# Kernel optimization log

Hardware: AMD Instinct MI355X
Metric: run time of the kernel (lower is better)

## Reference

```python
import jax, jax.numpy as jnp
import numpy as np
import math

# static config
NH, HD, HID = 16, 128, 2048
ROT = 64            # head_dim * partial_rotary_factor(0.5)
EPS = 1e-6
GROUPS = 8
CHUNK = 64
THETA = 10000.0
LAYER_IDX, N_LAYERS = 1, 32
B, S = 2, 2048


def _base_slopes(n):
    # power-of-two branch of HF ALiBi slopes
    start = 2 ** (-(2 ** (-(math.log2(n) - 3))))
    return [start * (start ** i) for i in range(n)]

# per-head log-decay (negative): slope = -base * (1 - (l-1)/(L-1) + 1e-5)
SLOPE = jnp.asarray(
    -np.array(_base_slopes(NH), dtype=np.float32)
    * (1.0 - (LAYER_IDX - 1) / (N_LAYERS - 1) + 1e-5),
    dtype=jnp.float32)  # [NH]


def _rmsnorm(x, w):
    return x * jax.lax.rsqrt(jnp.mean(x * x, axis=-1, keepdims=True) + EPS) * w


def _partial_rope(x, positions):
    # x: [B,S,NH,HD]; neox-style rotary on first ROT dims, rest passthrough
    half = ROT // 2
    inv_freq = 1.0 / (THETA ** (jnp.arange(half, dtype=jnp.float32) / half))
    ang = positions.astype(jnp.float32)[:, None] * inv_freq       # [S, half]
    cos = jnp.cos(ang)[None, :, None, :]
    sin = jnp.sin(ang)[None, :, None, :]
    x1, x2, rest = x[..., :half], x[..., half:ROT], x[..., ROT:]
    return jnp.concatenate(
        [x1 * cos - x2 * sin, x2 * cos + x1 * sin, rest], axis=-1)


def setup_inputs() -> dict:
    key = jax.random.key(0)
    ks = jax.random.split(key, 4)
    return {
        'positions': jnp.arange(S, dtype=jnp.int32),
        'hidden_states': jax.random.normal(ks[0], (B, S, HID), jnp.float32),
        'recurrent_state': jnp.zeros((B, NH, HD, HD), jnp.float32),
        'w_qkv': jax.random.normal(ks[1], (HID, 3 * NH * HD), jnp.float32) * 0.02,
        'w_g': jax.random.normal(ks[2], (HID, NH * HD), jnp.float32) * 0.02,
        'w_dense': jax.random.normal(ks[3], (NH * HD, HID), jnp.float32) * 0.02,
        'q_norm_w': jnp.ones((HD,), jnp.float32),
        'k_norm_w': jnp.ones((HD,), jnp.float32),
        'g_norm_w': jnp.ones((NH * HD,), jnp.float32),
    }


def reference(positions, hidden_states, recurrent_state, w_qkv, w_g, w_dense,
              q_norm_w, k_norm_w, g_norm_w):
    # fused QKV projection
    qkv = hidden_states @ w_qkv                       # [B,S,3*NH*HD]
    q, k, v = jnp.split(qkv, 3, axis=-1)
    q = q.reshape(B, S, NH, HD)
    k = k.reshape(B, S, NH, HD)
    v = v.reshape(B, S, NH, HD)

    # QK RMSNorm then partial rotary
    q = _partial_rope(_rmsnorm(q, q_norm_w), positions)
    k = _partial_rope(_rmsnorm(k, k_norm_w), positions)

    # chunked ALiBi-decayed linear attention:
    #   S_t = lam * S_{t-1} + k_t v_t^T ; o_t = q_t S_t, lam = exp(slope)
    NC = S // CHUNK
    qc = q.reshape(B, NC, CHUNK, NH, HD).transpose(1, 0, 3, 2, 4)  # [NC,B,NH,C,HD]
    kc = k.reshape(B, NC, CHUNK, NH, HD).transpose(1, 0, 3, 2, 4)
    vc = v.reshape(B, NC, CHUNK, NH, HD).transpose(1, 0, 3, 2, 4)

    t = jnp.arange(CHUNK, dtype=jnp.float32)
    # intra-chunk causal decay mask lam^(i-j), i>=j: [NH,C,C]
    dec_mask = jnp.where(t[:, None] >= t[None, :],
                         jnp.exp(SLOPE[:, None, None] * (t[:, None] - t[None, :])),
                         0.0)
    q_dec = jnp.exp(SLOPE[:, None] * (t[None, :] + 1.0))            # [NH,C] lam^(i+1)
    k_dec = jnp.exp(SLOPE[:, None] * (CHUNK - 1.0 - t[None, :]))    # [NH,C] lam^(C-1-j)
    lam_C = jnp.exp(SLOPE * CHUNK)                                   # [NH]

    def step(state, inp):
        qb, kb, vb = inp                                  # [B,NH,C,HD]
        scores = jnp.einsum('bhid,bhjd->bhij', qb, kb) * dec_mask[None]
        o_intra = jnp.einsum('bhij,bhjd->bhid', scores, vb)
        o_inter = jnp.einsum('bhid,bhde->bhie', qb * q_dec[None, :, :, None], state)
        new_state = (state * lam_C[None, :, None, None]
                     + jnp.einsum('bhjd,bhje->bhde', kb * k_dec[None, :, :, None], vb))
        return new_state, o_intra + o_inter

    _, o = jax.lax.scan(step, recurrent_state, (qc, kc, vc))  # o: [NC,B,NH,C,HD]
    o = o.transpose(1, 0, 3, 2, 4).reshape(B, S, NH * HD)

    # GroupRMSNorm on attention output, sigmoid gate, output projection
    og = o.reshape(B, S, GROUPS, (NH * HD) // GROUPS)
    og = og * jax.lax.rsqrt(jnp.mean(og * og, axis=-1, keepdims=True) + EPS)
    o = og.reshape(B, S, NH * HD) * g_norm_w
    o = o * jax.nn.sigmoid(hidden_states @ w_g)
    return o @ w_dense
```

## Files before the change

### kernel.cpp

```cpp
#include <hip/hip_runtime.h>
#include <hip/hip_bf16.h>
#include <math.h>

#define NH   16
#define HD   128
#define HID  2048
#define NKV  6144
#define B_   2
#define S_   2048
#define NC   32
#define CHUNK_ 64
#define GROUPS_ 8

typedef __bf16 bf16_t;
typedef bf16_t bf16x8 __attribute__((ext_vector_type(8)));
typedef float  f32x4  __attribute__((ext_vector_type(4)));

__device__ __forceinline__ float b2f(unsigned int u) {
    union { unsigned int u; float f; } c; c.u = (u & 0xffffu) << 16; return c.f;
}
__device__ __forceinline__ unsigned int f2b(float f) {
    union { float f; unsigned int u; } c; c.f = f;
    unsigned int u = c.u;
    return (u + 0x7fffu + ((u >> 16) & 1u)) >> 16;
}

#define GLOAD_LDS16(gp, lp) __builtin_amdgcn_global_load_lds(                     \
    (const __attribute__((address_space(1))) void*)(gp),                          \
    (__attribute__((address_space(3))) void*)(lp), 16, 0, 0)

__global__ __launch_bounds__(256) void cvt_bf16(const float* __restrict__ in,
                                                unsigned short* __restrict__ out, int n8)
{
    int i = blockIdx.x * 256 + threadIdx.x;
    if (i >= n8) return;
    const float4* p = (const float4*)in + (size_t)i * 2;
    float4 a = p[0], b = p[1];
    uint4 o;
    o.x = f2b(a.x) | (f2b(a.y) << 16);
    o.y = f2b(a.z) | (f2b(a.w) << 16);
    o.z = f2b(b.x) | (f2b(b.y) << 16);
    o.w = f2b(b.z) | (f2b(b.w) << 16);
    ((uint4*)out)[i] = o;
}

__global__ __launch_bounds__(256) void transpose_cvt(const float* __restrict__ in,
                                                     unsigned short* __restrict__ out,
                                                     int Kdim, int Ndim)
{
    __shared__ float tile[32][33];
    int ntx = Ndim >> 5;
    int bx = blockIdx.x % ntx;
    int by = blockIdx.x / ntx;
    int lx = threadIdx.x & 31, ly = threadIdx.x >> 5;
    int r0 = by * 32, c0 = bx * 32;
    #pragma unroll
    for (int r = 0; r < 4; ++r)
        tile[ly + r * 8][lx] = in[(size_t)(r0 + ly + r * 8) * Ndim + c0 + lx];
    __syncthreads();
    #pragma unroll
    for (int r = 0; r < 4; ++r)
        out[(size_t)(c0 + ly + r * 8) * Kdim + r0 + lx] = (unsigned short)f2b(tile[lx][ly + r * 8]);
}

__global__ __launch_bounds__(256) void pack_b(const float* __restrict__ in,
                                              unsigned short* __restrict__ out, int Ndim)
{
    __shared__ float tile[32][33];
    int ntx = Ndim >> 5;
    int bx = blockIdx.x % ntx;
    int by = blockIdx.x / ntx;
    int lx = threadIdx.x & 31, ly = threadIdx.x >> 5;
    int r0 = by * 32, c0 = bx * 32;
    #pragma unroll
    for (int r = 0; r < 4; ++r)
        tile[ly + r * 8][lx] = in[(size_t)(r0 + ly + r * 8) * Ndim + c0 + lx];
    __syncthreads();
    int quad = (lx >> 3) & 3;
    int e    = lx & 7;
    #pragma unroll
    for (int r = 0; r < 4; ++r) {
        int n = c0 + ly + r * 8;
        int n16 = n >> 4, l16 = n & 15;
        out[((size_t)(n16 * 64 + by) << 9) + (quad * 16 + l16) * 8 + e] =
            (unsigned short)f2b(tile[lx][ly + r * 8]);
    }
}


__device__ __forceinline__ void ld_fr4(bf16x8 (&d)[4][2], const bf16_t* b, int s0, int ri) {
    #pragma unroll
    for (int i = 0; i < 4; ++i)
        #pragma unroll
        for (int k = 0; k < 2; ++k)
            d[i][k] = *(const bf16x8*)(b + (((s0 + i) * 2 + k) << 9) + ri);
}
__device__ __forceinline__ void mfma_quad(f32x4 (&a)[4][2], const bf16x8 (&af)[4][2],
                                          const bf16x8 (&bv)[2][2]) {
    #pragma unroll
    for (int mt = 0; mt < 4; ++mt)
        #pragma unroll
        for (int nt = 0; nt < 2; ++nt)
            #pragma unroll
            for (int ks = 0; ks < 2; ++ks)
                a[mt][nt] = __builtin_amdgcn_mfma_f32_16x16x32_bf16(af[mt][ks], bv[nt][ks], a[mt][nt], 0, 0, 0);
}
__device__ __forceinline__ void load_bfrag(bf16x8 (&d)[2][2][2], const bf16_t* Bp,
                                           int n16b, int tt, int lane8) {
    #pragma unroll
    for (int nh = 0; nh < 2; ++nh)
        #pragma unroll
        for (int nt = 0; nt < 2; ++nt)
            #pragma unroll
            for (int ks = 0; ks < 2; ++ks)
                d[nh][nt][ks] = *(const bf16x8*)(Bp +
                    ((size_t)((n16b + nh * 8 + nt) * 64 + tt * 2 + ks) << 9) + lane8);
}

#define BAR()     asm volatile("s_barrier" ::: "memory")
#define VMCNT0()  asm volatile("s_waitcnt vmcnt(0)" ::: "memory")

__global__ __launch_bounds__(512, 2) void gemm_qg_256(const bf16_t* __restrict__ A,
                                                      const bf16_t* __restrict__ Bp,
                                                      unsigned short* __restrict__ Cq,
                                                      unsigned short* __restrict__ Cg)
{
    __shared__ bf16_t Asm[2][2][8192];
    const int K  = HID;
    const int NT = K / 64;

    int tid  = threadIdx.x;
    int wave = tid >> 6, lane = tid & 63;
    int wm = wave >> 2, wn = wave & 3;
    int l16 = lane & 15, quad = lane >> 4;
    int wm4 = wm * 4;
    int lane8 = lane * 8;

    int bid = blockIdx.x;
    int xcd = bid & 7, idx = bid >> 3;
    int by  = (xcd >> 2) * 8 + (idx >> 3);
    int bx  = (xcd & 3) * 8 + (idx & 7);

    int n16b = bx * 16 + wn * 2;

    int rd_in = ((l16 << 5) | (quad << 3)) ^ (((l16 >> 3) & 1) << 4);

    int ch = lane ^ ((lane & 32) >> 4);
    int rr = ch >> 2;
    int cc = (ch & 3) * 8;

    const bf16_t* aSrc0 = A + (size_t)(by * 256 +       wave * 16 + rr) * K + cc;
    const bf16_t* aSrc1 = A + (size_t)(by * 256 + 128 + wave * 16 + rr) * K + cc;

#define STAGE_A(h, t) do {                                                        \
        const bf16_t* _g = ((h) ? aSrc1 : aSrc0) + (size_t)(t) * 64;              \
        bf16_t* _l = &Asm[(t) & 1][(h)][wave * 1024 + lane * 8];                  \
        GLOAD_LDS16(_g,      _l);                                                 \
        GLOAD_LDS16(_g + 32, _l + 512); } while (0)

    f32x4 acc[2][2][4][2];
    #pragma unroll
    for (int a0 = 0; a0 < 2; ++a0)
        #pragma unroll
        for (int a1 = 0; a1 < 2; ++a1)
            #pragma unroll
            for (int a2 = 0; a2 < 4; ++a2)
                #pragma unroll
                for (int a3 = 0; a3 < 2; ++a3) { f32x4 z = {0.f,0.f,0.f,0.f}; acc[a0][a1][a2][a3] = z; }

    bf16x8 af[4][2];
    bf16x8 bfA[2][2][2], bfB[2][2][2];

    load_bfrag(bfA, Bp, n16b, 0, lane8);
    STAGE_A(0, 0); STAGE_A(1, 0);
    VMCNT0();
    BAR();

#define QG_TILE(t, BFC, BFN) do {                                                 \
        const int buf_ = (t) & 1;                                                 \
        load_bfrag(BFN, Bp, n16b, (t) + 1, lane8);                                \
        STAGE_A(0, (t) + 1); STAGE_A(1, (t) + 1);                                 \
        ld_fr4(af, &Asm[buf_][0][0], wm4, rd_in);                                 \
        mfma_quad(acc[0][0], af, BFC[0]);                                         \
        mfma_quad(acc[0][1], af, BFC[1]);                                         \
        ld_fr4(af, &Asm[buf_][1][0], wm4, rd_in);                                 \
        mfma_quad(acc[1][1], af, BFC[1]);                                         \
        mfma_quad(acc[1][0], af, BFC[0]);                                         \
        VMCNT0();                                                                 \
        BAR(); } while (0)

    for (int t = 0; t < NT - 2; t += 2) {
        QG_TILE(t,     bfA, bfB);
        QG_TILE(t + 1, bfB, bfA);
    }
    QG_TILE(NT - 2, bfA, bfB);
    {
        ld_fr4(af, &Asm[1][0][0], wm4, rd_in);
        mfma_quad(acc[0][0], af, bfB[0]);
        mfma_quad(acc[0][1], af, bfB[1]);
        ld_fr4(af, &Asm[1][1][0], wm4, rd_in);
        mfma_quad(acc[1][1], af, bfB[1]);
        mfma_quad(acc[1][0], af, bfB[0]);
    }
#undef QG_TILE
#undef STAGE_A

    unsigned short* Cc; int Nn, colbase;
    if (bx < 24) { Cc = Cq; Nn = NKV; colbase = bx * 256; }
    else         { Cc = Cg; Nn = HID; colbase = bx * 256 - NKV; }
    int row0 = by * 256 + wm * 64 + quad * 4;
    int col0 = colbase + wn * 32 + l16;
    #pragma unroll
    for (int mh = 0; mh < 2; ++mh)
        #pragma unroll
        for (int nh = 0; nh < 2; ++nh)
            #pragma unroll
            for (int mt = 0; mt < 4; ++mt)
                #pragma unroll
                for (int nt = 0; nt < 2; ++nt) {
                    int col = col0 + nh * 128 + nt * 16;
                    #pragma unroll
                    for (int r = 0; r < 4; ++r) {
                        int row = row0 + mh * 128 + mt * 16 + r;
                        Cc[(size_t)row * Nn + col] = (unsigned short)f2b(acc[mh][nh][mt][nt][r]);
                    }
                }
}

__global__ __launch_bounds__(256, 2) void gemm_out_128(const bf16_t* __restrict__ A,
                                                       const bf16_t* __restrict__ Bt,
                                                       float* __restrict__ C)
{
    __shared__ bf16_t As[2][4096];
    __shared__ bf16_t Bs[2][4096];
    const int K  = HID;
    const int NT = K / 32;

    int tid  = threadIdx.x;
    int wave = tid >> 6, lane = tid & 63;
    int wm2 = wave >> 1, wn2 = wave & 1;
    int l16 = lane & 15, quad = lane >> 4;
    int w2 = wave * 2;

    int bid = blockIdx.x;
    int xcd = bid & 7, idx = bid >> 3;
    int by  = (xcd >> 1) * 8 + (idx >> 3);
    int bx  = (xcd & 1) * 8 + (idx & 7);

    int rd_in = ((l16 << 5) | (quad << 3)) ^ (((l16 >> 3) & 1) << 4);
    int ch = lane ^ ((lane & 32) >> 4);
    int rr = ch >> 2;
    int cc = (ch & 3) * 8;

    const bf16_t* aSrc = A  + (size_t)(by * 128 + w2 * 16 + rr) * K + cc;
    const bf16_t* bSrc = Bt + (size_t)(bx * 128 + w2 * 16 + rr) * K + cc;

#define OSTAGE(t) do {                                                            \
        const int nb_ = (t) & 1;                                                  \
        const bf16_t* _ga = aSrc + (size_t)(t) * 32;                              \
        const bf16_t* _gb = bSrc + (size_t)(t) * 32;                              \
        GLOAD_LDS16(_ga,                  &As[nb_][w2 * 512 + lane * 8]);         \
        GLOAD_LDS16(_ga + (size_t)16 * K, &As[nb_][w2 * 512 + 512 + lane * 8]);   \
        GLOAD_LDS16(_gb,                  &Bs[nb_][w2 * 512 + lane * 8]);         \
        GLOAD_LDS16(_gb + (size_t)16 * K, &Bs[nb_][w2 * 512 + 512 + lane * 8]); } while (0)

    f32x4 acc[4][4];
    #pragma unroll
    for (int i = 0; i < 4; ++i)
        #pragma unroll
        for (int j = 0; j < 4; ++j) { f32x4 z = {0.f,0.f,0.f,0.f}; acc[i][j] = z; }

#define OCOMP(t) do {                                                             \
        const int b_ = (t) & 1;                                                   \
        bf16x8 af_[4], bf_[4];                                                    \
        _Pragma("unroll")                                                         \
        for (int i = 0; i < 4; ++i)                                               \
            af_[i] = *(const bf16x8*)(&As[b_][((wm2 * 4 + i) << 9) + rd_in]);     \
        _Pragma("unroll")                                                         \
        for (int j = 0; j < 4; ++j)                                               \
            bf_[j] = *(const bf16x8*)(&Bs[b_][((wn2 * 4 + j) << 9) + rd_in]);     \
        _Pragma("unroll")                                                         \
        for (int i = 0; i < 4; ++i)                                               \
            _Pragma("unroll")                                                     \
            for (int j = 0; j < 4; ++j)                                           \
                acc[i][j] = __builtin_amdgcn_mfma_f32_16x16x32_bf16(af_[i], bf_[j], acc[i][j], 0, 0, 0); } while (0)

    OSTAGE(0);
    VMCNT0();
    BAR();
    #pragma unroll 2
    for (int t = 0; t < NT - 1; ++t) {
        OSTAGE(t + 1);
        OCOMP(t);
        VMCNT0();
        BAR();
    }
    OCOMP(NT - 1);
#undef OSTAGE
#undef OCOMP

    #pragma unroll
    for (int i = 0; i < 4; ++i)
        #pragma unroll
        for (int j = 0; j < 4; ++j) {
            int col = bx * 128 + wn2 * 64 + j * 16 + l16;
            #pragma unroll
            for (int r = 0; r < 4; ++r) {
                int row = by * 128 + wm2 * 64 + i * 16 + quad * 4 + r;
                C[(size_t)row * HID + col] = acc[i][j][r];
            }
        }
}

__global__ __launch_bounds__(256) void norm_rope(unsigned short* __restrict__ qkv,
                                                 const int* __restrict__ positions,
                                                 const float* __restrict__ qw,
                                                 const float* __restrict__ kw)
{
    int bs = blockIdx.x;
    int s  = bs & (S_ - 1);
    int tid = threadIdx.x;
    int l16 = tid & 15;
    unsigned short* base = qkv + (size_t)bs * NKV;
    float pos = (float)positions[s];

    #pragma unroll
    for (int p = 0; p < 2; ++p) {
        int rr = p * 16 + (tid >> 4);
        int qk = rr >> 4;
        int h  = rr & 15;
        unsigned short* row = base + qk * HID + h * HD;
        const float* w = qk ? kw : qw;
        uint4 v = *(const uint4*)(row + l16 * 8);
        float x[8];
        x[0] = b2f(v.x); x[1] = b2f(v.x >> 16);
        x[2] = b2f(v.y); x[3] = b2f(v.y >> 16);
        x[4] = b2f(v.z); x[5] = b2f(v.z >> 16);
        x[6] = b2f(v.w); x[7] = b2f(v.w >> 16);
        float ss = 0.f;
        #pragma unroll
        for (int t = 0; t < 8; ++t) ss += x[t] * x[t];
        ss += __shfl_xor(ss, 1); ss += __shfl_xor(ss, 2);
        ss += __shfl_xor(ss, 4); ss += __shfl_xor(ss, 8);
        float inv = rsqrtf(ss * (1.0f / 128.0f) + 1e-6f);
        float n[8];
        #pragma unroll
        for (int t = 0; t < 8; ++t) n[t] = x[t] * inv * w[l16 * 8 + t];
        float pr[8];
        #pragma unroll
        for (int t = 0; t < 8; ++t) pr[t] = __shfl_xor(n[t], 4);
        if (l16 < 8) {
            #pragma unroll
            for (int t = 0; t < 8; ++t) {
                int dim = l16 * 8 + t;
                int i = dim & 31;
                float ang = pos * exp2f(-(float)i * 0.4152410118609203f);
                float cs = cosf(ang), sn = sinf(ang);
                n[t] = (dim < 32) ? (n[t] * cs - pr[t] * sn) : (n[t] * cs + pr[t] * sn);
            }
        }
        uint4 o;
        o.x = f2b(n[0]) | (f2b(n[1]) << 16);
        o.y = f2b(n[2]) | (f2b(n[3]) << 16);
        o.z = f2b(n[4]) | (f2b(n[5]) << 16);
        o.w = f2b(n[6]) | (f2b(n[7]) << 16);
        *(uint4*)(row + l16 * 8) = o;
    }
}

__global__ __launch_bounds__(256) void chunk_kv(const unsigned short* __restrict__ qkv,
                                                unsigned short* __restrict__ wbuf)
{
    __shared__ unsigned short kt[128 * 72];
    __shared__ unsigned short vt[128 * 72];
    int bi = blockIdx.x;
    int c = bi & 31, bh = bi >> 5, h = bh & 15, b = bh >> 4;
    int tid = threadIdx.x;
    float slope = -exp2f(-0.5f * (float)(h + 1)) * (1.0f + 1e-5f);

    const unsigned short* kbase = qkv + ((size_t)(b * S_ + c * CHUNK_)) * NKV + HID + h * HD;
    const unsigned short* vbase = kbase + HID;

    for (int idx = tid; idx < 4096; idx += 256) {
        int j = idx >> 6, p = idx & 63;
        unsigned int ku = *(const unsigned int*)(kbase + (size_t)j * NKV + p * 2);
        kt[(2 * p) * 72 + j]     = (unsigned short)(ku & 0xffffu);
        kt[(2 * p + 1) * 72 + j] = (unsigned short)(ku >> 16);
        float kd = expf(slope * (float)(63 - j));
        unsigned int vu = *(const unsigned int*)(vbase + (size_t)j * NKV + p * 2);
        vt[(2 * p) * 72 + j]     = (unsigned short)f2b(b2f(vu) * kd);
        vt[(2 * p + 1) * 72 + j] = (unsigned short)f2b(b2f(vu >> 16) * kd);
    }
    __syncthreads();

    int lane = tid & 63, wave = tid >> 6;
    int wm = (wave >> 1) * 64;
    int wn = (wave & 1) * 64;
    int l16 = lane & 15, quad = lane >> 4;

    f32x4 acc[4][4];
    #pragma unroll
    for (int i = 0; i < 4; ++i)
        #pragma unroll
        for (int j = 0; j < 4; ++j) { f32x4 z = {0.f,0.f,0.f,0.f}; acc[i][j] = z; }

    #pragma unroll
    for (int ks = 0; ks < 64; ks += 32) {
        bf16x8 af[4], bf[4];
        #pragma unroll
        for (int t = 0; t < 4; ++t) {
            af[t] = *(const bf16x8*)((const bf16_t*)vt + (wm + t * 16 + l16) * 72 + ks + quad * 8);
            bf[t] = *(const bf16x8*)((const bf16_t*)kt + (wn + t * 16 + l16) * 72 + ks + quad * 8);
        }
        #pragma unroll
        for (int mt = 0; mt < 4; ++mt)
            #pragma unroll
            for (int nt = 0; nt < 4; ++nt)
                acc[mt][nt] = __builtin_amdgcn_mfma_f32_16x16x32_bf16(af[mt], bf[nt], acc[mt][nt], 0, 0, 0);
    }

    unsigned short* wp = wbuf + ((size_t)bi << 14);
    #pragma unroll
    for (int mt = 0; mt < 4; ++mt)
        #pragma unroll
        for (int nt = 0; nt < 4; ++nt) {
            int dcol = wn + nt * 16 + l16;
            #pragma unroll
            for (int r = 0; r < 4; ++r) {
                int erow = wm + mt * 16 + quad * 4 + r;
                wp[(size_t)erow * 128 + dcol] = (unsigned short)f2b(acc[mt][nt][r]);
            }
        }
}

__global__ __launch_bounds__(256) void state_scan(const unsigned short* __restrict__ wbuf,
                                                  const float* __restrict__ rs0,
                                                  unsigned short* __restrict__ stbuf)
{
    int bi = blockIdx.x;
    int es = bi & 15, bh = bi >> 4, h = bh & 15, b = bh >> 4;
    int tid = threadIdx.x;
    float slope = -exp2f(-0.5f * (float)(h + 1)) * (1.0f + 1e-5f);
    float lam = expf(slope * 64.0f);

    int e  = es * 8 + (tid >> 5);
    int d0 = (tid & 31) * 4;

    float S[4];
    const float* rp = rs0 + ((size_t)(b * NH + h)) * HD * HD + e;
    #pragma unroll
    for (int t = 0; t < 4; ++t) S[t] = rp[(size_t)(d0 + t) * HD];

    size_t off = (size_t)e * 128 + d0;
    size_t base = (((size_t)bh * NC) << 14) + off;
    uint2 w0 = *(const uint2*)(wbuf + base);
    uint2 w1 = *(const uint2*)(wbuf + base + (1 << 14));
    for (int c = 0; c < NC; ++c) {
        uint2 o;
        o.x = f2b(S[0]) | (f2b(S[1]) << 16);
        o.y = f2b(S[2]) | (f2b(S[3]) << 16);
        *(uint2*)(stbuf + base) = o;
        uint2 w2 = w1;
        if (c + 2 < NC) w2 = *(const uint2*)(wbuf + base + (2 << 14));
        S[0] = S[0] * lam + b2f(w0.x);
        S[1] = S[1] * lam + b2f(w0.x >> 16);
        S[2] = S[2] * lam + b2f(w0.y);
        S[3] = S[3] * lam + b2f(w0.y >> 16);
        w0 = w1; w1 = w2;
        base += (1 << 14);
    }
}

__global__ __launch_bounds__(256) void chunk_out(const unsigned short* __restrict__ qkv,
                                                 const unsigned short* __restrict__ stbuf,
                                                 unsigned short* __restrict__ obuf)
{
    __shared__ unsigned short qs[64 * 136];
    __shared__ unsigned short vt[128 * 72];
    __shared__ unsigned short sc[64 * 72];

    int bi = blockIdx.x;
    int c = bi & 31, bh = bi >> 5, h = bh & 15, b = bh >> 4;
    int tid = threadIdx.x;
    float slope = -exp2f(-0.5f * (float)(h + 1)) * (1.0f + 1e-5f);

    int lane = tid & 63, wave = tid >> 6;
    int l16 = lane & 15, quad = lane >> 4;
    int wn3 = wave * 32;

    const unsigned short* stp = stbuf + (((size_t)bh * NC + c) << 14);
    bf16x8 bsf[4][2];
    #pragma unroll
    for (int ksp4 = 0; ksp4 < 4; ++ksp4)
        #pragma unroll
        for (int nt = 0; nt < 2; ++nt)
            bsf[ksp4][nt] = *(const bf16x8*)((const bf16_t*)stp +
                (size_t)(wn3 + nt * 16 + l16) * 128 + ksp4 * 32 + quad * 8);

    const unsigned short* qrow = qkv + ((size_t)(b * S_ + c * CHUNK_)) * NKV + h * HD;
    const unsigned short* krow = qrow + HID;
    for (int idx = tid; idx < 1024; idx += 256) {
        int row = idx >> 4, c8 = (idx & 15) * 8;
        *(uint4*)(qs + row * 136 + c8) = *(const uint4*)(qrow + (size_t)row * NKV + c8);
    }
    const unsigned short* vbase = qrow + 2 * HID;
    for (int idx = tid; idx < 4096; idx += 256) {
        int j = idx >> 6, p = idx & 63;
        unsigned int vu = *(const unsigned int*)(vbase + (size_t)j * NKV + p * 2);
        vt[(2 * p) * 72 + j]     = (unsigned short)(vu & 0xffffu);
        vt[(2 * p + 1) * 72 + j] = (unsigned short)(vu >> 16);
    }
    __syncthreads();

    {
        f32x4 accS[4];
        #pragma unroll
        for (int t = 0; t < 4; ++t) { f32x4 z = {0.f,0.f,0.f,0.f}; accS[t] = z; }
        #pragma unroll
        for (int ksp = 0; ksp < 128; ksp += 32) {
            bf16x8 aq = *(const bf16x8*)((const bf16_t*)qs + (wave * 16 + l16) * 136 + ksp + quad * 8);
            #pragma unroll
            for (int nt = 0; nt < 4; ++nt) {
                bf16x8 bk = *(const bf16x8*)((const bf16_t*)krow + (size_t)(nt * 16 + l16) * NKV + ksp + quad * 8);
                accS[nt] = __builtin_amdgcn_mfma_f32_16x16x32_bf16(aq, bk, accS[nt], 0, 0, 0);
            }
        }
        float ad[4];
        #pragma unroll
        for (int r = 0; r < 4; ++r) ad[r] = expf(slope * (float)(wave * 16 + quad * 4 + r));
        #pragma unroll
        for (int nt = 0; nt < 4; ++nt) {
            int j = nt * 16 + l16;
            float bd = expf(-slope * (float)j);
            #pragma unroll
            for (int r = 0; r < 4; ++r) {
                int i = wave * 16 + quad * 4 + r;
                float v = (i >= j) ? accS[nt][r] * ad[r] * bd : 0.0f;
                sc[i * 72 + j] = (unsigned short)f2b(v);
            }
        }
    }
    __syncthreads();

    f32x4 accI[4][2], accE[4][2];
    #pragma unroll
    for (int i = 0; i < 4; ++i)
        #pragma unroll
        for (int j = 0; j < 2; ++j) { f32x4 z = {0.f,0.f,0.f,0.f}; accI[i][j] = z; accE[i][j] = z; }

    #pragma unroll
    for (int ksp = 0; ksp < 64; ksp += 32) {
        bf16x8 as[4], bv[2];
        #pragma unroll
        for (int mt = 0; mt < 4; ++mt)
            as[mt] = *(const bf16x8*)((const bf16_t*)sc + (mt * 16 + l16) * 72 + ksp + quad * 8);
        #pragma unroll
        for (int nt = 0; nt < 2; ++nt)
            bv[nt] = *(const bf16x8*)((const bf16_t*)vt + (wn3 + nt * 16 + l16) * 72 + ksp + quad * 8);
        #pragma unroll
        for (int mt = 0; mt < 4; ++mt)
            #pragma unroll
            for (int nt = 0; nt < 2; ++nt)
                accI[mt][nt] = __builtin_amdgcn_mfma_f32_16x16x32_bf16(as[mt], bv[nt], accI[mt][nt], 0, 0, 0);
    }
    #pragma unroll
    for (int ksp4 = 0; ksp4 < 4; ++ksp4) {
        bf16x8 aq[4];
        #pragma unroll
        for (int mt = 0; mt < 4; ++mt)
            aq[mt] = *(const bf16x8*)((const bf16_t*)qs + (mt * 16 + l16) * 136 + ksp4 * 32 + quad * 8);
        #pragma unroll
        for (int mt = 0; mt < 4; ++mt)
            #pragma unroll
            for (int nt = 0; nt < 2; ++nt)
                accE[mt][nt] = __builtin_amdgcn_mfma_f32_16x16x32_bf16(aq[mt], bsf[ksp4][nt], accE[mt][nt], 0, 0, 0);
    }

    #pragma unroll
    for (int mt = 0; mt < 4; ++mt) {
        #pragma unroll
        for (int r = 0; r < 4; ++r) {
            int i = mt * 16 + quad * 4 + r;
            float qd = expf(slope * (float)(i + 1));
            int orow = b * S_ + c * CHUNK_ + i;
            #pragma unroll
            for (int nt = 0; nt < 2; ++nt) {
                int col = h * HD + wn3 + nt * 16 + l16;
                float o = accI[mt][nt][r] + qd * accE[mt][nt][r];
                obuf[(size_t)orow * 2048 + col] = (unsigned short)f2b(o);
            }
        }
    }
}

__global__ __launch_bounds__(256) void gnorm_gate(const unsigned short* __restrict__ o,
                                                  unsigned short* __restrict__ gate,
                                                  const float* __restrict__ gw)
{
    int row = blockIdx.x >> 3;
    int g   = blockIdx.x & 7;
    int col = g * 256 + threadIdx.x;
    size_t idx = (size_t)row * 2048 + col;
    float ov = b2f(o[idx]);
    float ss = ov * ov;
    #pragma unroll
    for (int off = 32; off > 0; off >>= 1) ss += __shfl_xor(ss, off);
    __shared__ float part[4];
    if ((threadIdx.x & 63) == 0) part[threadIdx.x >> 6] = ss;
    __syncthreads();
    float tot = part[0] + part[1] + part[2] + part[3];
    float inv = rsqrtf(tot * (1.0f / 256.0f) + 1e-6f);
    float gv = b2f(gate[idx]);
    float sig = 1.0f / (1.0f + expf(-gv));
    gate[idx] = (unsigned short)f2b(ov * inv * gw[col] * sig);
}

extern "C" void kernel_launch(void* const* d_in, const int* in_sizes, int n_in,
                              void* d_out, int out_size, void* d_ws, size_t ws_size,
                              hipStream_t stream) {
    const int*   positions = (const int*)d_in[0];
    const float* hidden    = (const float*)d_in[1];
    const float* rstate    = (const float*)d_in[2];
    const float* w_qkv     = (const float*)d_in[3];
    const float* w_g       = (const float*)d_in[4];
    const float* w_dense   = (const float*)d_in[5];
    const float* q_norm_w  = (const float*)d_in[6];
    const float* k_norm_w  = (const float*)d_in[7];
    const float* g_norm_w  = (const float*)d_in[8];
    float* out = (float*)d_out;

    const int MR = B_ * S_;

    char* w = (char*)d_ws;
    unsigned short* qkv  = (unsigned short*)w;            w += (size_t)MR * NKV * 2;
    unsigned short* gbuf = (unsigned short*)w;            w += (size_t)MR * 2048 * 2;
    unsigned short* wdT  = (unsigned short*)w;            w += (size_t)HID * HID * 2;
    char* regionA = w;                                    w += (size_t)MR * HID * 2 + (size_t)8192 * HID * 2;
    char* regionB = w;
    unsigned short* hbf   = (unsigned short*)regionA;
    unsigned short* Bp    = (unsigned short*)(regionA + (size_t)MR * HID * 2);
    unsigned short* stbuf = (unsigned short*)regionA;
    unsigned short* wbuf  = (unsigned short*)regionB;
    unsigned short* obuf  = (unsigned short*)regionB;

    cvt_bf16<<<dim3((MR * HID / 8 + 255) / 256), dim3(256), 0, stream>>>(hidden, hbf, MR * HID / 8);
    pack_b<<<dim3((HID / 32) * (NKV / 32)), dim3(256), 0, stream>>>(w_qkv, Bp, NKV);
    pack_b<<<dim3((HID / 32) * (HID / 32)), dim3(256), 0, stream>>>(w_g, Bp + (size_t)384 * 64 * 512, HID);
    transpose_cvt<<<dim3((HID / 32) * (HID / 32)), dim3(256), 0, stream>>>(w_dense, wdT, HID, HID);

    gemm_qg_256<<<dim3(512), dim3(512), 0, stream>>>(
        (const bf16_t*)hbf, (const bf16_t*)Bp, qkv, gbuf);
    norm_rope<<<dim3(B_ * S_), dim3(256), 0, stream>>>(qkv, positions, q_norm_w, k_norm_w);

    chunk_kv<<<dim3(B_ * NH * NC), dim3(256), 0, stream>>>(qkv, wbuf);
    state_scan<<<dim3(B_ * NH * 16), dim3(256), 0, stream>>>(wbuf, rstate, stbuf);
    chunk_out<<<dim3(B_ * NH * NC), dim3(256), 0, stream>>>(qkv, stbuf, obuf);

    gnorm_gate<<<dim3(MR * GROUPS_), dim3(256), 0, stream>>>(obuf, gbuf, g_norm_w);
    gemm_out_128<<<dim3(512), dim3(256), 0, stream>>>(
        (const bf16_t*)gbuf, (const bf16_t*)wdT, out);
}
```

Baseline: 436.5 us.

## Stage GEMM B operand through LDS and cache K chunk in shared memory

The QKV/gate GEMM now loads the B operand (a transposed bf16 weight) into double-buffered LDS with async global-to-LDS copies, the same way as A, instead of each wave loading pre-packed B fragments straight from global memory into registers. The custom pack_b layout is replaced by a plain transpose_cvt. In chunk_out, the K tile is also copied into shared memory rather than read directly from global per MFMA. This doubles LDS use in the GEMM (64KB per block), which may reduce occupancy at two blocks per CU, and adds LDS read traffic.

```diff
diff --git a/kernel.cpp b/kernel.cpp
--- a/kernel.cpp
+++ b/kernel.cpp
@@ -63,30 +63,6 @@
         out[(size_t)(c0 + ly + r * 8) * Kdim + r0 + lx] = (unsigned short)f2b(tile[lx][ly + r * 8]);
 }
 
-__global__ __launch_bounds__(256) void pack_b(const float* __restrict__ in,
-                                              unsigned short* __restrict__ out, int Ndim)
-{
-    __shared__ float tile[32][33];
-    int ntx = Ndim >> 5;
-    int bx = blockIdx.x % ntx;
-    int by = blockIdx.x / ntx;
-    int lx = threadIdx.x & 31, ly = threadIdx.x >> 5;
-    int r0 = by * 32, c0 = bx * 32;
-    #pragma unroll
-    for (int r = 0; r < 4; ++r)
-        tile[ly + r * 8][lx] = in[(size_t)(r0 + ly + r * 8) * Ndim + c0 + lx];
-    __syncthreads();
-    int quad = (lx >> 3) & 3;
-    int e    = lx & 7;
-    #pragma unroll
-    for (int r = 0; r < 4; ++r) {
-        int n = c0 + ly + r * 8;
-        int n16 = n >> 4, l16 = n & 15;
-        out[((size_t)(n16 * 64 + by) << 9) + (quad * 16 + l16) * 8 + e] =
-            (unsigned short)f2b(tile[lx][ly + r * 8]);
-    }
-}
-
 
 __device__ __forceinline__ void ld_fr4(bf16x8 (&d)[4][2], const bf16_t* b, int s0, int ri) {
     #pragma unroll
@@ -95,6 +71,13 @@
         for (int k = 0; k < 2; ++k)
             d[i][k] = *(const bf16x8*)(b + (((s0 + i) * 2 + k) << 9) + ri);
 }
+__device__ __forceinline__ void ld_fr2(bf16x8 (&d)[2][2], const bf16_t* b, int s0, int ri) {
+    #pragma unroll
+    for (int i = 0; i < 2; ++i)
+        #pragma unroll
+        for (int k = 0; k < 2; ++k)
+            d[i][k] = *(const bf16x8*)(b + (((s0 + i) * 2 + k) << 9) + ri);
+}
 __device__ __forceinline__ void mfma_quad(f32x4 (&a)[4][2], const bf16x8 (&af)[4][2],
                                           const bf16x8 (&bv)[2][2]) {
     #pragma unroll
@@ -105,27 +88,17 @@
             for (int ks = 0; ks < 2; ++ks)
                 a[mt][nt] = __builtin_amdgcn_mfma_f32_16x16x32_bf16(af[mt][ks], bv[nt][ks], a[mt][nt], 0, 0, 0);
 }
-__device__ __forceinline__ void load_bfrag(bf16x8 (&d)[2][2][2], const bf16_t* Bp,
-                                           int n16b, int tt, int lane8) {
-    #pragma unroll
-    for (int nh = 0; nh < 2; ++nh)
-        #pragma unroll
-        for (int nt = 0; nt < 2; ++nt)
-            #pragma unroll
-            for (int ks = 0; ks < 2; ++ks)
-                d[nh][nt][ks] = *(const bf16x8*)(Bp +
-                    ((size_t)((n16b + nh * 8 + nt) * 64 + tt * 2 + ks) << 9) + lane8);
-}
 
 #define BAR()     asm volatile("s_barrier" ::: "memory")
 #define VMCNT0()  asm volatile("s_waitcnt vmcnt(0)" ::: "memory")
 
 __global__ __launch_bounds__(512, 2) void gemm_qg_256(const bf16_t* __restrict__ A,
-                                                      const bf16_t* __restrict__ Bp,
+                                                      const bf16_t* __restrict__ Bt,
                                                       unsigned short* __restrict__ Cq,
                                                       unsigned short* __restrict__ Cg)
 {
     __shared__ bf16_t Asm[2][2][8192];
+    __shared__ bf16_t Bsm[2][2][8192];
     const int K  = HID;
     const int NT = K / 64;
 
@@ -133,30 +106,34 @@
     int wave = tid >> 6, lane = tid & 63;
     int wm = wave >> 2, wn = wave & 3;
     int l16 = lane & 15, quad = lane >> 4;
-    int wm4 = wm * 4;
-    int lane8 = lane * 8;
+    int wm4 = wm * 4, wn2 = wn * 2;
 
     int bid = blockIdx.x;
     int xcd = bid & 7, idx = bid >> 3;
     int by  = (xcd >> 2) * 8 + (idx >> 3);
     int bx  = (xcd & 3) * 8 + (idx & 7);
 
-    int n16b = bx * 16 + wn * 2;
-
     int rd_in = ((l16 << 5) | (quad << 3)) ^ (((l16 >> 3) & 1) << 4);
 
     int ch = lane ^ ((lane & 32) >> 4);
     int rr = ch >> 2;
     int cc = (ch & 3) * 8;
 
-    const bf16_t* aSrc0 = A + (size_t)(by * 256 +       wave * 16 + rr) * K + cc;
-    const bf16_t* aSrc1 = A + (size_t)(by * 256 + 128 + wave * 16 + rr) * K + cc;
+    const bf16_t* aSrc0 = A  + (size_t)(by * 256 +       wave * 16 + rr) * K + cc;
+    const bf16_t* aSrc1 = A  + (size_t)(by * 256 + 128 + wave * 16 + rr) * K + cc;
+    const bf16_t* bSrc0 = Bt + (size_t)(bx * 256 +       wave * 16 + rr) * K + cc;
+    const bf16_t* bSrc1 = Bt + (size_t)(bx * 256 + 128 + wave * 16 + rr) * K + cc;
 
 #define STAGE_A(h, t) do {                                                        \
         const bf16_t* _g = ((h) ? aSrc1 : aSrc0) + (size_t)(t) * 64;              \
         bf16_t* _l = &Asm[(t) & 1][(h)][wave * 1024 + lane * 8];                  \
         GLOAD_LDS16(_g,      _l);                                                 \
         GLOAD_LDS16(_g + 32, _l + 512); } while (0)
+#define STAGE_B(h, t) do {                                                        \
+        const bf16_t* _g = ((h) ? bSrc1 : bSrc0) + (size_t)(t) * 64;              \
+        bf16_t* _l = &Bsm[(t) & 1][(h)][wave * 1024 + lane * 8];                  \
+        GLOAD_LDS16(_g,      _l);                                                 \
+        GLOAD_LDS16(_g + 32, _l + 512); } while (0)
 
     f32x4 acc[2][2][4][2];
     #pragma unroll
@@ -168,42 +145,42 @@
                 #pragma unroll
                 for (int a3 = 0; a3 < 2; ++a3) { f32x4 z = {0.f,0.f,0.f,0.f}; acc[a0][a1][a2][a3] = z; }
 
-    bf16x8 af[4][2];
-    bf16x8 bfA[2][2][2], bfB[2][2][2];
-
-    load_bfrag(bfA, Bp, n16b, 0, lane8);
-    STAGE_A(0, 0); STAGE_A(1, 0);
+    STAGE_A(0, 0); STAGE_B(0, 0); STAGE_A(1, 0); STAGE_B(1, 0);
     VMCNT0();
     BAR();
 
-#define QG_TILE(t, BFC, BFN) do {                                                 \
-        const int buf_ = (t) & 1;                                                 \
-        load_bfrag(BFN, Bp, n16b, (t) + 1, lane8);                                \
-        STAGE_A(0, (t) + 1); STAGE_A(1, (t) + 1);                                 \
-        ld_fr4(af, &Asm[buf_][0][0], wm4, rd_in);                                 \
-        mfma_quad(acc[0][0], af, BFC[0]);                                         \
-        mfma_quad(acc[0][1], af, BFC[1]);                                         \
-        ld_fr4(af, &Asm[buf_][1][0], wm4, rd_in);                                 \
-        mfma_quad(acc[1][1], af, BFC[1]);                                         \
-        mfma_quad(acc[1][0], af, BFC[0]);                                         \
-        VMCNT0();                                                                 \
-        BAR(); } while (0)
-
-    for (int t = 0; t < NT - 2; t += 2) {
-        QG_TILE(t,     bfA, bfB);
-        QG_TILE(t + 1, bfB, bfA);
-    }
-    QG_TILE(NT - 2, bfA, bfB);
+    #pragma unroll 2
+    for (int t = 0; t < NT - 1; ++t) {
+        const int buf = t & 1;
+        STAGE_A(0, t + 1); STAGE_B(0, t + 1); STAGE_A(1, t + 1); STAGE_B(1, t + 1);
+        {
+            bf16x8 afA[4][2], afB[4][2], bf0[2][2], bf1[2][2];
+            ld_fr4(afA, &Asm[buf][0][0], wm4, rd_in);
+            ld_fr2(bf0, &Bsm[buf][0][0], wn2, rd_in);
+            mfma_quad(acc[0][0], afA, bf0);
+            ld_fr2(bf1, &Bsm[buf][1][0], wn2, rd_in);
+            mfma_quad(acc[0][1], afA, bf1);
+            ld_fr4(afB, &Asm[buf][1][0], wm4, rd_in);
+            mfma_quad(acc[1][1], afB, bf1);
+            mfma_quad(acc[1][0], afB, bf0);
+        }
+        VMCNT0();
+        BAR();
+    }
     {
-        ld_fr4(af, &Asm[1][0][0], wm4, rd_in);
-        mfma_quad(acc[0][0], af, bfB[0]);
-        mfma_quad(acc[0][1], af, bfB[1]);
-        ld_fr4(af, &Asm[1][1][0], wm4, rd_in);
-        mfma_quad(acc[1][1], af, bfB[1]);
-        mfma_quad(acc[1][0], af, bfB[0]);
-    }
-#undef QG_TILE
+        const int buf = (NT - 1) & 1;
+        bf16x8 afA[4][2], afB[4][2], bf0[2][2], bf1[2][2];
+        ld_fr4(afA, &Asm[buf][0][0], wm4, rd_in);
+        ld_fr2(bf0, &Bsm[buf][0][0], wn2, rd_in);
+        mfma_quad(acc[0][0], afA, bf0);
+        ld_fr2(bf1, &Bsm[buf][1][0], wn2, rd_in);
+        mfma_quad(acc[0][1], afA, bf1);
+        ld_fr4(afB, &Asm[buf][1][0], wm4, rd_in);
+        mfma_quad(acc[1][1], afB, bf1);
+        mfma_quad(acc[1][0], afB, bf0);
+    }
 #undef STAGE_A
+#undef STAGE_B
 
     unsigned short* Cc; int Nn, colbase;
     if (bx < 24) { Cc = Cq; Nn = NKV; colbase = bx * 256; }
@@ -476,6 +453,7 @@
                                                  unsigned short* __restrict__ obuf)
 {
     __shared__ unsigned short qs[64 * 136];
+    __shared__ unsigned short kss[64 * 136];
     __shared__ unsigned short vt[128 * 72];
     __shared__ unsigned short sc[64 * 72];
 
@@ -501,7 +479,8 @@
     const unsigned short* krow = qrow + HID;
     for (int idx = tid; idx < 1024; idx += 256) {
         int row = idx >> 4, c8 = (idx & 15) * 8;
-        *(uint4*)(qs + row * 136 + c8) = *(const uint4*)(qrow + (size_t)row * NKV + c8);
+        *(uint4*)(qs  + row * 136 + c8) = *(const uint4*)(qrow + (size_t)row * NKV + c8);
+        *(uint4*)(kss + row * 136 + c8) = *(const uint4*)(krow + (size_t)row * NKV + c8);
     }
     const unsigned short* vbase = qrow + 2 * HID;
     for (int idx = tid; idx < 4096; idx += 256) {
@@ -521,7 +500,7 @@
             bf16x8 aq = *(const bf16x8*)((const bf16_t*)qs + (wave * 16 + l16) * 136 + ksp + quad * 8);
             #pragma unroll
             for (int nt = 0; nt < 4; ++nt) {
-                bf16x8 bk = *(const bf16x8*)((const bf16_t*)krow + (size_t)(nt * 16 + l16) * NKV + ksp + quad * 8);
+                bf16x8 bk = *(const bf16x8*)((const bf16_t*)kss + (nt * 16 + l16) * 136 + ksp + quad * 8);
                 accS[nt] = __builtin_amdgcn_mfma_f32_16x16x32_bf16(aq, bk, accS[nt], 0, 0, 0);
             }
         }
@@ -638,18 +617,20 @@
     char* regionA = w;                                    w += (size_t)MR * HID * 2 + (size_t)8192 * HID * 2;
     char* regionB = w;
     unsigned short* hbf   = (unsigned short*)regionA;
-    unsigned short* Bp    = (unsigned short*)(regionA + (size_t)MR * HID * 2);
+    unsigned short* btQG  = (unsigned short*)(regionA + (size_t)MR * HID * 2);
+    unsigned short* wqT   = btQG;
+    unsigned short* wgT   = btQG + (size_t)NKV * HID;
     unsigned short* stbuf = (unsigned short*)regionA;
     unsigned short* wbuf  = (unsigned short*)regionB;
     unsigned short* obuf  = (unsigned short*)regionB;
 
     cvt_bf16<<<dim3((MR * HID / 8 + 255) / 256), dim3(256), 0, stream>>>(hidden, hbf, MR * HID / 8);
-    pack_b<<<dim3((HID / 32) * (NKV / 32)), dim3(256), 0, stream>>>(w_qkv, Bp, NKV);
-    pack_b<<<dim3((HID / 32) * (HID / 32)), dim3(256), 0, stream>>>(w_g, Bp + (size_t)384 * 64 * 512, HID);
+    transpose_cvt<<<dim3((HID / 32) * (NKV / 32)), dim3(256), 0, stream>>>(w_qkv, wqT, HID, NKV);
+    transpose_cvt<<<dim3((HID / 32) * (HID / 32)), dim3(256), 0, stream>>>(w_g, wgT, HID, HID);
     transpose_cvt<<<dim3((HID / 32) * (HID / 32)), dim3(256), 0, stream>>>(w_dense, wdT, HID, HID);
 
     gemm_qg_256<<<dim3(512), dim3(512), 0, stream>>>(
-        (const bf16_t*)hbf, (const bf16_t*)Bp, qkv, gbuf);
+        (const bf16_t*)hbf, (const bf16_t*)btQG, qkv, gbuf);
     norm_rope<<<dim3(B_ * S_), dim3(256), 0, stream>>>(qkv, positions, q_norm_w, k_norm_w);
 
     chunk_kv<<<dim3(B_ * NH * NC), dim3(256), 0, stream>>>(qkv, wbuf);
```

Result: faster. 424.1 us (-2.8%).
